# Performance work log

Hardware: AMD Instinct MI355X
Metric: run time of the kernel (lower is better)

## Reference

```python
import jax, jax.numpy as jnp
import numpy as np

TEMPERATURE = 0.07
EPS = 1e-8  # torch cosine_similarity eps


def setup_inputs() -> dict:
    key = jax.random.key(0)
    k1, k2 = jax.random.split(key)
    N, D = 8192, 256
    u = jax.random.normal(k1, (N, D), dtype=jnp.float32)
    v = jax.random.normal(k2, (N, D), dtype=jnp.float32)
    return {"u": u, "v": v}


def reference(u, v):
    # cosine similarity = (u/|u|) @ (v/|v|)^T ; torch clamps norms at eps
    un = u / jnp.maximum(jnp.linalg.norm(u, axis=-1, keepdims=True), EPS)
    vn = v / jnp.maximum(jnp.linalg.norm(v, axis=-1, keepdims=True), EPS)
    logits = jnp.einsum('nd,md->nm', un, vn) / TEMPERATURE  # [N, N]
    # cross-entropy with labels = arange(N): mean(logsumexp(row) - diag)
    lse = jax.scipy.special.logsumexp(logits, axis=-1)  # [N]
    diag = jnp.diagonal(logits)
    return jnp.mean(lse - diag)
```

## Files before the change

kernel.cpp:

```cpp
#include <hip/hip_runtime.h>
#include <hip/hip_bf16.h>
#include <math.h>

#define NROWS 8192
#define DIM   256
#define INV_T 14.285714285714286f
#define LOG2E_T 20.60992893360759f
#define EPS_N 1e-8f

typedef __attribute__((ext_vector_type(8))) short short8;
typedef __attribute__((ext_vector_type(4))) float f32x4;

typedef const __attribute__((address_space(1))) void g_void;
typedef __attribute__((address_space(3))) void l_void;

__device__ inline unsigned short f2bf(float x) {
    __hip_bfloat16 h = __float2bfloat16(x);
    return __builtin_bit_cast(unsigned short, h);
}

__global__ __launch_bounds__(256) void norm_kernel(
    const float* __restrict__ u, const float* __restrict__ v,
    unsigned short* __restrict__ un, unsigned short* __restrict__ vn,
    float* __restrict__ diag, float* __restrict__ rowsum)
{
    if (threadIdx.x < 4) rowsum[blockIdx.x * 4 + threadIdx.x] = 0.0f;

    const int wid  = threadIdx.x >> 6;
    const int lane = threadIdx.x & 63;
    const int r    = blockIdx.x * 4 + wid;

    const float4* u4 = (const float4*)(u + (size_t)r * DIM);
    const float4* v4 = (const float4*)(v + (size_t)r * DIM);
    float4 a = u4[lane];
    float4 b = v4[lane];

    float ssu = a.x * a.x + a.y * a.y + a.z * a.z + a.w * a.w;
    float ssv = b.x * b.x + b.y * b.y + b.z * b.z + b.w * b.w;
    float duv = a.x * b.x + a.y * b.y + a.z * b.z + a.w * b.w;

    #pragma unroll
    for (int m = 32; m >= 1; m >>= 1) {
        ssu += __shfl_xor(ssu, m);
        ssv += __shfl_xor(ssv, m);
        duv += __shfl_xor(duv, m);
    }

    const float iu  = 1.0f / fmaxf(sqrtf(ssu), EPS_N);
    const float iv  = 1.0f / fmaxf(sqrtf(ssv), EPS_N);
    const float ius = iu * LOG2E_T;

    ushort4 pu, pv;
    pu.x = f2bf(a.x * ius); pu.y = f2bf(a.y * ius);
    pu.z = f2bf(a.z * ius); pu.w = f2bf(a.w * ius);
    pv.x = f2bf(b.x * iv);  pv.y = f2bf(b.y * iv);
    pv.z = f2bf(b.z * iv);  pv.w = f2bf(b.w * iv);
    *(ushort4*)(un + (size_t)r * DIM + 4 * lane) = pu;
    *(ushort4*)(vn + (size_t)r * DIM + 4 * lane) = pv;

    if (lane == 0) diag[r] = duv * iu * iv * INV_T;
}

__global__ __launch_bounds__(256, 2)
void gemm_kernel(
    const unsigned short* __restrict__ un, const unsigned short* __restrict__ vn,
    float* __restrict__ rowsum)
{
    __shared__ unsigned short Bs[2][32][64][8];

    const int t    = threadIdx.x;
    const int lane = t & 63;
    const int wid  = t >> 6;
    const int wr   = wid >> 1;
    const int wc   = wid & 1;
    const int bid  = blockIdx.x;
    const int by   = bid & 7;
    const int bx   = bid >> 3;
    const int i0   = bx * 128;
    const int j0   = by * 1024;

    const int lr = lane & 15;
    const int lg = lane >> 4;

    auto stage = [&](int buf, int jt) {
        #pragma unroll
        for (int s = 0; s < 8; ++s) {
            const int kg = wid * 8 + s;
            const unsigned short* src = vn + (size_t)(jt + lane) * DIM + kg * 8;
            __builtin_amdgcn_global_load_lds((g_void*)src,
                (l_void*)&Bs[buf][kg][0][0], 16, 0, 0);
        }
    };

    stage(0, j0);

    short8 av[4][8];
    #pragma unroll
    for (int m = 0; m < 4; ++m) {
        const unsigned short* ar =
            un + (size_t)(i0 + wr * 64 + m * 16 + lr) * DIM + lg * 8;
        #pragma unroll
        for (int k = 0; k < 8; ++k) {
            av[m][k] = *(const short8*)(ar + k * 32);
            asm volatile("" : "+a"(av[m][k]));
        }
    }

    float rs[4][4] = {};

    __syncthreads();

    int buf = 0;
    #pragma unroll 1
    for (int js = 0; js < 16; ++js) {
        if (js < 15) stage(buf ^ 1, j0 + (js + 1) * 64);

        f32x4 acc[4][2];
        #pragma unroll
        for (int k = 0; k < 8; ++k) {
            const short8 b0 = *(const short8*)&Bs[buf][k * 4 + lg][wc * 32 + lr][0];
            const short8 b1 = *(const short8*)&Bs[buf][k * 4 + lg][wc * 32 + 16 + lr][0];
            if (k == 0) {
                const f32x4 z = {0.f, 0.f, 0.f, 0.f};
                #pragma unroll
                for (int m = 0; m < 4; ++m) {
                    acc[m][0] = __builtin_amdgcn_mfma_f32_16x16x32_bf16(av[m][0], b0, z, 0, 0, 0);
                    acc[m][1] = __builtin_amdgcn_mfma_f32_16x16x32_bf16(av[m][0], b1, z, 0, 0, 0);
                }
            } else {
                #pragma unroll
                for (int m = 0; m < 4; ++m) {
                    acc[m][0] = __builtin_amdgcn_mfma_f32_16x16x32_bf16(av[m][k], b0, acc[m][0], 0, 0, 0);
                    acc[m][1] = __builtin_amdgcn_mfma_f32_16x16x32_bf16(av[m][k], b1, acc[m][1], 0, 0, 0);
                }
            }
        }

        #pragma unroll
        for (int m = 0; m < 4; ++m)
            #pragma unroll
            for (int n = 0; n < 2; ++n)
                #pragma unroll
                for (int r = 0; r < 4; ++r)
                    rs[m][r] += __builtin_amdgcn_exp2f(acc[m][n][r]);

        __syncthreads();
        buf ^= 1;
    }

    #pragma unroll
    for (int m = 0; m < 4; ++m)
        #pragma unroll
        for (int r = 0; r < 4; ++r) {
            float s = rs[m][r];
            s += __shfl_xor(s, 1);
            s += __shfl_xor(s, 2);
            s += __shfl_xor(s, 4);
            s += __shfl_xor(s, 8);
            if (lr == 0)
                atomicAdd(&rowsum[i0 + wr * 64 + m * 16 + lg * 4 + r], s);
        }
}

__global__ __launch_bounds__(1024) void finish_kernel(
    const float* __restrict__ rowsum, const float* __restrict__ diag,
    float* __restrict__ out)
{
    __shared__ float red[16];
    const int t    = threadIdx.x;
    const int lane = t & 63;
    const int wid  = t >> 6;

    float c = 0.0f;
    #pragma unroll
    for (int q = 0; q < 8; ++q) {
        const int r = t + 1024 * q;
        c += logf(rowsum[r]) - diag[r];
    }
    #pragma unroll
    for (int m = 32; m >= 1; m >>= 1) c += __shfl_xor(c, m);
    if (lane == 0) red[wid] = c;
    __syncthreads();
    if (t == 0) {
        float s = 0.0f;
        #pragma unroll
        for (int k = 0; k < 16; ++k) s += red[k];
        out[0] = s * (1.0f / (float)NROWS);
    }
}

extern "C" void kernel_launch(void* const* d_in, const int* in_sizes, int n_in,
                              void* d_out, int out_size, void* d_ws, size_t ws_size,
                              hipStream_t stream)
{
    const float* u = (const float*)d_in[0];
    const float* v = (const float*)d_in[1];
    float* out = (float*)d_out;

    char* w = (char*)d_ws;
    unsigned short* un = (unsigned short*)w;
    unsigned short* vn = (unsigned short*)(w + (size_t)NROWS * DIM * 2);
    float* diag   = (float*)(w + (size_t)NROWS * DIM * 4);
    float* rowsum = diag + NROWS;

    norm_kernel<<<NROWS / 4, 256, 0, stream>>>(u, v, un, vn, diag, rowsum);
    gemm_kernel<<<512, 256, 0, stream>>>(un, vn, rowsum);
    finish_kernel<<<1, 1024, 0, stream>>>(rowsum, diag, out);
}
```

Measured before the change: 119.0 us.

## Halve GEMM column tile, double grid with XCD-aware mapping, parallelize final reduction

The GEMM's per-step B tile shrinks from 64 to 32 columns and each block covers 512 columns instead of 1024. The grid doubles to 1024 blocks, with a block-to-XCD mapping that groups row halves and column quarters per XCD for L2 locality. The occupancy hint rises to 4 blocks per CU. The finish kernel now runs 32 blocks that combine through an atomic add into a memset output, replacing the single-block reduction. The trade-off is less MFMA work per LDS load and per barrier, and a float atomic sum whose order can vary between runs.

```diff
diff --git a/kernel.cpp b/kernel.cpp
--- a/kernel.cpp
+++ b/kernel.cpp
@@ -61,12 +61,12 @@
     if (lane == 0) diag[r] = duv * iu * iv * INV_T;
 }
 
-__global__ __launch_bounds__(256, 2)
+__global__ __launch_bounds__(256, 4)
 void gemm_kernel(
     const unsigned short* __restrict__ un, const unsigned short* __restrict__ vn,
     float* __restrict__ rowsum)
 {
-    __shared__ unsigned short Bs[2][32][64][8];
+    __shared__ unsigned short Bs[2][32][32][8];
 
     const int t    = threadIdx.x;
     const int lane = t & 63;
@@ -74,21 +74,27 @@
     const int wr   = wid >> 1;
     const int wc   = wid & 1;
     const int bid  = blockIdx.x;
-    const int by   = bid & 7;
-    const int bx   = bid >> 3;
-    const int i0   = bx * 128;
-    const int j0   = by * 1024;
+
+    const int xcd = bid & 7;
+    const int loc = bid >> 3;
+    const int ih  = xcd >> 2;
+    const int jq  = xcd & 3;
+    const int bx  = loc & 31;
+    const int jp  = loc >> 5;
+    const int i0  = (ih * 32 + bx) * 128;
+    const int j0  = (jq * 4 + jp) * 512;
 
     const int lr = lane & 15;
     const int lg = lane >> 4;
 
     auto stage = [&](int buf, int jt) {
         #pragma unroll
-        for (int s = 0; s < 8; ++s) {
-            const int kg = wid * 8 + s;
-            const unsigned short* src = vn + (size_t)(jt + lane) * DIM + kg * 8;
+        for (int s = 0; s < 4; ++s) {
+            const int bkg = wid * 8 + s * 2;
+            const unsigned short* src =
+                vn + (size_t)(jt + (lane & 31)) * DIM + (bkg + (lane >> 5)) * 8;
             __builtin_amdgcn_global_load_lds((g_void*)src,
-                (l_void*)&Bs[buf][kg][0][0], 16, 0, 0);
+                (l_void*)&Bs[buf][bkg][0][0], 16, 0, 0);
         }
     };
 
@@ -113,36 +119,29 @@
     int buf = 0;
     #pragma unroll 1
     for (int js = 0; js < 16; ++js) {
-        if (js < 15) stage(buf ^ 1, j0 + (js + 1) * 64);
-
-        f32x4 acc[4][2];
+        if (js < 15) stage(buf ^ 1, j0 + (js + 1) * 32);
+
+        f32x4 acc[4];
         #pragma unroll
         for (int k = 0; k < 8; ++k) {
-            const short8 b0 = *(const short8*)&Bs[buf][k * 4 + lg][wc * 32 + lr][0];
-            const short8 b1 = *(const short8*)&Bs[buf][k * 4 + lg][wc * 32 + 16 + lr][0];
+            const short8 b = *(const short8*)&Bs[buf][k * 4 + lg][wc * 16 + lr][0];
             if (k == 0) {
                 const f32x4 z = {0.f, 0.f, 0.f, 0.f};
                 #pragma unroll
-                for (int m = 0; m < 4; ++m) {
-                    acc[m][0] = __builtin_amdgcn_mfma_f32_16x16x32_bf16(av[m][0], b0, z, 0, 0, 0);
-                    acc[m][1] = __builtin_amdgcn_mfma_f32_16x16x32_bf16(av[m][0], b1, z, 0, 0, 0);
-                }
+                for (int m = 0; m < 4; ++m)
+                    acc[m] = __builtin_amdgcn_mfma_f32_16x16x32_bf16(av[m][0], b, z, 0, 0, 0);
             } else {
                 #pragma unroll
-                for (int m = 0; m < 4; ++m) {
-                    acc[m][0] = __builtin_amdgcn_mfma_f32_16x16x32_bf16(av[m][k], b0, acc[m][0], 0, 0, 0);
-                    acc[m][1] = __builtin_amdgcn_mfma_f32_16x16x32_bf16(av[m][k], b1, acc[m][1], 0, 0, 0);
-                }
+                for (int m = 0; m < 4; ++m)
+                    acc[m] = __builtin_amdgcn_mfma_f32_16x16x32_bf16(av[m][k], b, acc[m], 0, 0, 0);
             }
         }
 
         #pragma unroll
         for (int m = 0; m < 4; ++m)
             #pragma unroll
-            for (int n = 0; n < 2; ++n)
-                #pragma unroll
-                for (int r = 0; r < 4; ++r)
-                    rs[m][r] += __builtin_amdgcn_exp2f(acc[m][n][r]);
+            for (int r = 0; r < 4; ++r)
+                rs[m][r] += __builtin_amdgcn_exp2f(acc[m][r]);
 
         __syncthreads();
         buf ^= 1;
@@ -162,30 +161,24 @@
         }
 }
 
-__global__ __launch_bounds__(1024) void finish_kernel(
+__global__ __launch_bounds__(256) void finish_kernel(
     const float* __restrict__ rowsum, const float* __restrict__ diag,
     float* __restrict__ out)
 {
-    __shared__ float red[16];
+    __shared__ float red[4];
     const int t    = threadIdx.x;
     const int lane = t & 63;
     const int wid  = t >> 6;
-
-    float c = 0.0f;
-    #pragma unroll
-    for (int q = 0; q < 8; ++q) {
-        const int r = t + 1024 * q;
-        c += logf(rowsum[r]) - diag[r];
-    }
+    const int r    = blockIdx.x * 256 + t;
+
+    float c = logf(rowsum[r]) - diag[r];
     #pragma unroll
     for (int m = 32; m >= 1; m >>= 1) c += __shfl_xor(c, m);
     if (lane == 0) red[wid] = c;
     __syncthreads();
     if (t == 0) {
-        float s = 0.0f;
-        #pragma unroll
-        for (int k = 0; k < 16; ++k) s += red[k];
-        out[0] = s * (1.0f / (float)NROWS);
+        float s = red[0] + red[1] + red[2] + red[3];
+        atomicAdd(out, s * (1.0f / (float)NROWS));
     }
 }
 
@@ -203,7 +196,8 @@
     float* diag   = (float*)(w + (size_t)NROWS * DIM * 4);
     float* rowsum = diag + NROWS;
 
+    hipMemsetAsync(out, 0, sizeof(float), stream);
     norm_kernel<<<NROWS / 4, 256, 0, stream>>>(u, v, un, vn, diag, rowsum);
-    gemm_kernel<<<512, 256, 0, stream>>>(un, vn, rowsum);
-    finish_kernel<<<1, 1024, 0, stream>>>(rowsum, diag, out);
-}
+    gemm_kernel<<<1024, 256, 0, stream>>>(un, vn, rowsum);
+    finish_kernel<<<NROWS / 256, 256, 0, stream>>>(rowsum, diag, out);
+}
```

New measurement: 229.9 us. 93.3% more time.

## Fuse normalize, GEMM and final reduction into one persistent kernel with grid barrier

Applied to the files above, without the earlier changes.

Merges the three launches into one kernel. Each block first normalizes 16 rows, then all blocks wait at a software grid-wide barrier built on a global atomic counter. After that the GEMM/exp-sum runs as before, and the last block to finish, found with a second atomic counter, does the log/diag reduction. This removes two kernel launches and their gaps, but adds a memset, a spin barrier that assumes all 512 blocks are co-resident, and a serial tail reduction done by a single block. It also drops the unroll-1 pragma on the main loop.

```diff
diff --git a/kernel.cpp b/kernel.cpp
--- a/kernel.cpp
+++ b/kernel.cpp
@@ -7,6 +7,7 @@
 #define INV_T 14.285714285714286f
 #define LOG2E_T 20.60992893360759f
 #define EPS_N 1e-8f
+#define GRID 512
 
 typedef __attribute__((ext_vector_type(8))) short short8;
 typedef __attribute__((ext_vector_type(4))) float f32x4;
@@ -19,66 +20,85 @@
     return __builtin_bit_cast(unsigned short, h);
 }
 
-__global__ __launch_bounds__(256) void norm_kernel(
-    const float* __restrict__ u, const float* __restrict__ v,
-    unsigned short* __restrict__ un, unsigned short* __restrict__ vn,
-    float* __restrict__ diag, float* __restrict__ rowsum)
-{
-    if (threadIdx.x < 4) rowsum[blockIdx.x * 4 + threadIdx.x] = 0.0f;
-
-    const int wid  = threadIdx.x >> 6;
-    const int lane = threadIdx.x & 63;
-    const int r    = blockIdx.x * 4 + wid;
-
-    const float4* u4 = (const float4*)(u + (size_t)r * DIM);
-    const float4* v4 = (const float4*)(v + (size_t)r * DIM);
-    float4 a = u4[lane];
-    float4 b = v4[lane];
-
-    float ssu = a.x * a.x + a.y * a.y + a.z * a.z + a.w * a.w;
-    float ssv = b.x * b.x + b.y * b.y + b.z * b.z + b.w * b.w;
-    float duv = a.x * b.x + a.y * b.y + a.z * b.z + a.w * b.w;
-
-    #pragma unroll
-    for (int m = 32; m >= 1; m >>= 1) {
-        ssu += __shfl_xor(ssu, m);
-        ssv += __shfl_xor(ssv, m);
-        duv += __shfl_xor(duv, m);
-    }
-
-    const float iu  = 1.0f / fmaxf(sqrtf(ssu), EPS_N);
-    const float iv  = 1.0f / fmaxf(sqrtf(ssv), EPS_N);
-    const float ius = iu * LOG2E_T;
-
-    ushort4 pu, pv;
-    pu.x = f2bf(a.x * ius); pu.y = f2bf(a.y * ius);
-    pu.z = f2bf(a.z * ius); pu.w = f2bf(a.w * ius);
-    pv.x = f2bf(b.x * iv);  pv.y = f2bf(b.y * iv);
-    pv.z = f2bf(b.z * iv);  pv.w = f2bf(b.w * iv);
-    *(ushort4*)(un + (size_t)r * DIM + 4 * lane) = pu;
-    *(ushort4*)(vn + (size_t)r * DIM + 4 * lane) = pv;
-
-    if (lane == 0) diag[r] = duv * iu * iv * INV_T;
-}
-
 __global__ __launch_bounds__(256, 2)
-void gemm_kernel(
-    const unsigned short* __restrict__ un, const unsigned short* __restrict__ vn,
-    float* __restrict__ rowsum)
+void fused_kernel(const float* __restrict__ u, const float* __restrict__ v,
+                  unsigned short* __restrict__ un, unsigned short* __restrict__ vn,
+                  float* __restrict__ diag, float* __restrict__ rowsum,
+                  unsigned int* __restrict__ bar, unsigned int* __restrict__ fin,
+                  float* __restrict__ out)
 {
     __shared__ unsigned short Bs[2][32][64][8];
+    __shared__ float red[4];
+    __shared__ unsigned int lastflag;
 
     const int t    = threadIdx.x;
     const int lane = t & 63;
     const int wid  = t >> 6;
-    const int wr   = wid >> 1;
-    const int wc   = wid & 1;
     const int bid  = blockIdx.x;
-    const int by   = bid & 7;
-    const int bx   = bid >> 3;
-    const int i0   = bx * 128;
-    const int j0   = by * 1024;
-
+
+    {
+        const int r = bid * 16 + (t >> 4);
+        const int q = t & 15;
+        const float4* u4 = (const float4*)(u + (size_t)r * DIM);
+        const float4* v4 = (const float4*)(v + (size_t)r * DIM);
+        float4 a0 = u4[q], a1 = u4[q + 16], a2 = u4[q + 32], a3 = u4[q + 48];
+        float4 b0 = v4[q], b1 = v4[q + 16], b2 = v4[q + 32], b3 = v4[q + 48];
+
+        auto d4 = [](float4 p, float4 s) {
+            return p.x * s.x + p.y * s.y + p.z * s.z + p.w * s.w;
+        };
+        float ssu = d4(a0, a0) + d4(a1, a1) + d4(a2, a2) + d4(a3, a3);
+        float ssv = d4(b0, b0) + d4(b1, b1) + d4(b2, b2) + d4(b3, b3);
+        float duv = d4(a0, b0) + d4(a1, b1) + d4(a2, b2) + d4(a3, b3);
+
+        #pragma unroll
+        for (int m = 1; m <= 8; m <<= 1) {
+            ssu += __shfl_xor(ssu, m);
+            ssv += __shfl_xor(ssv, m);
+            duv += __shfl_xor(duv, m);
+        }
+
+        const float iu  = 1.0f / fmaxf(sqrtf(ssu), EPS_N);
+        const float iv  = 1.0f / fmaxf(sqrtf(ssv), EPS_N);
+        const float ius = iu * LOG2E_T;
+
+        auto pack = [](float4 x, float s) {
+            ushort4 p;
+            p.x = f2bf(x.x * s); p.y = f2bf(x.y * s);
+            p.z = f2bf(x.z * s); p.w = f2bf(x.w * s);
+            return p;
+        };
+        unsigned short* ur = un + (size_t)r * DIM;
+        unsigned short* vr = vn + (size_t)r * DIM;
+        *(ushort4*)(ur + q * 4)          = pack(a0, ius);
+        *(ushort4*)(ur + (q + 16) * 4)   = pack(a1, ius);
+        *(ushort4*)(ur + (q + 32) * 4)   = pack(a2, ius);
+        *(ushort4*)(ur + (q + 48) * 4)   = pack(a3, ius);
+        *(ushort4*)(vr + q * 4)          = pack(b0, iv);
+        *(ushort4*)(vr + (q + 16) * 4)   = pack(b1, iv);
+        *(ushort4*)(vr + (q + 32) * 4)   = pack(b2, iv);
+        *(ushort4*)(vr + (q + 48) * 4)   = pack(b3, iv);
+        if (q == 0) diag[r] = duv * iu * iv * INV_T;
+    }
+
+    __threadfence();
+    __syncthreads();
+    if (t == 0) {
+        __hip_atomic_fetch_add(bar, 1u, __ATOMIC_ACQ_REL,
+                               __HIP_MEMORY_SCOPE_AGENT);
+        while (__hip_atomic_load(bar, __ATOMIC_ACQUIRE,
+                                 __HIP_MEMORY_SCOPE_AGENT) < GRID) {
+            __builtin_amdgcn_s_sleep(2);
+        }
+    }
+    __syncthreads();
+
+    const int by = bid & 7;
+    const int bx = bid >> 3;
+    const int i0 = bx * 128;
+    const int j0 = by * 1024;
+    const int wr = wid >> 1;
+    const int wc = wid & 1;
     const int lr = lane & 15;
     const int lg = lane >> 4;
 
@@ -111,7 +131,6 @@
     __syncthreads();
 
     int buf = 0;
-    #pragma unroll 1
     for (int js = 0; js < 16; ++js) {
         if (js < 15) stage(buf ^ 1, j0 + (js + 1) * 64);
 
@@ -160,32 +179,30 @@
             if (lr == 0)
                 atomicAdd(&rowsum[i0 + wr * 64 + m * 16 + lg * 4 + r], s);
         }
-}
-
-__global__ __launch_bounds__(1024) void finish_kernel(
-    const float* __restrict__ rowsum, const float* __restrict__ diag,
-    float* __restrict__ out)
-{
-    __shared__ float red[16];
-    const int t    = threadIdx.x;
-    const int lane = t & 63;
-    const int wid  = t >> 6;
-
-    float c = 0.0f;
-    #pragma unroll
-    for (int q = 0; q < 8; ++q) {
-        const int r = t + 1024 * q;
-        c += logf(rowsum[r]) - diag[r];
-    }
-    #pragma unroll
-    for (int m = 32; m >= 1; m >>= 1) c += __shfl_xor(c, m);
-    if (lane == 0) red[wid] = c;
+
+    __threadfence();
     __syncthreads();
     if (t == 0) {
-        float s = 0.0f;
-        #pragma unroll
-        for (int k = 0; k < 16; ++k) s += red[k];
-        out[0] = s * (1.0f / (float)NROWS);
+        unsigned int old = atomicAdd(fin, 1u);
+        lastflag = (old == GRID - 1) ? 1u : 0u;
+    }
+    __syncthreads();
+    if (lastflag) {
+        __threadfence();
+        float c = 0.0f;
+        #pragma unroll
+        for (int q = 0; q < NROWS / 256; ++q) {
+            const int r = t + 256 * q;
+            const float sv = __hip_atomic_load(&rowsum[r], __ATOMIC_RELAXED,
+                                               __HIP_MEMORY_SCOPE_AGENT);
+            c += logf(sv) - diag[r];
+        }
+        #pragma unroll
+        for (int m = 32; m >= 1; m >>= 1) c += __shfl_xor(c, m);
+        if (lane == 0) red[wid] = c;
+        __syncthreads();
+        if (t == 0)
+            out[0] = (red[0] + red[1] + red[2] + red[3]) * (1.0f / (float)NROWS);
     }
 }
 
@@ -202,8 +219,11 @@
     unsigned short* vn = (unsigned short*)(w + (size_t)NROWS * DIM * 2);
     float* diag   = (float*)(w + (size_t)NROWS * DIM * 4);
     float* rowsum = diag + NROWS;
-
-    norm_kernel<<<NROWS / 4, 256, 0, stream>>>(u, v, un, vn, diag, rowsum);
-    gemm_kernel<<<512, 256, 0, stream>>>(un, vn, rowsum);
-    finish_kernel<<<1, 1024, 0, stream>>>(rowsum, diag, out);
+    unsigned int* bar = (unsigned int*)(rowsum + NROWS);
+    unsigned int* fin = bar + 1;
+
+    hipMemsetAsync(rowsum, 0, NROWS * sizeof(float) + 2 * sizeof(unsigned int),
+                   stream);
+    fused_kernel<<<GRID, 256, 0, stream>>>(u, v, un, vn, diag, rowsum,
+                                           bar, fin, out);
 }
```

Result: slower. 227.5 us (+91.2%).
